# Kernel optimization log

Hardware: AMD Instinct MI355X
Metric: run time of the kernel (lower is better)

The kernel has to match this reference:

```python
import jax, jax.numpy as jnp
import numpy as np

K_SELECTED = 8  # config.num_selected_heads


def setup_inputs() -> dict:
    key = jax.random.key(0)
    k1, k2 = jax.random.split(key, 2)
    B, N, H, L = 4, 4096, 2048, 64
    x = jax.random.normal(k1, (B, N, H), dtype=jnp.float32)
    W_r = jax.random.normal(k2, (L, H), dtype=jnp.float32) * 0.02  # nn.Linear weight (L, H), no bias
    expert_bias = jnp.zeros((L,), dtype=jnp.float32)
    active_mask = jnp.ones((B, N), dtype=bool)
    return {"x": x, "W_r": W_r, "expert_bias": expert_bias, "active_mask": active_mask}


def reference(x, W_r, expert_bias, active_mask):
    L = expert_bias.shape[0]
    K = K_SELECTED
    # logits = x @ W_r.T  (bias-free routing projection)
    logits = jnp.einsum('bnh,lh->bnl', x, W_r)
    routing_scores = jax.nn.softmax(logits, axis=-1)            # unbiased probs
    biased_scores = jax.nn.softmax(logits + expert_bias, -1)    # biased probs for selection
    # top-K on biased scores -> selected head indices (B, N, K)
    _, selected_heads = jax.lax.top_k(biased_scores, K)
    # gather unbiased scores at selected indices and renormalize
    gathered = jnp.take_along_axis(routing_scores, selected_heads, axis=-1)
    routing_probs = gathered / gathered.sum(axis=-1, keepdims=True)
    # scatter into assignment mask: one-hot over L summed over K slots
    assignment_mask = jax.nn.one_hot(selected_heads, L, dtype=x.dtype).sum(axis=-2)  # (B, N, L)
    am = active_mask.astype(x.dtype)
    active_assignments = assignment_mask * am[..., None]
    num_active_assignments = am.sum() * K
    routing_freqs = active_assignments.sum(axis=(0, 1)) / num_active_assignments  # (L,)
    # LoadBalanceLoss.apply(expert_bias, routing_freqs): squared-imbalance value
    inv_L = 1.0 / L
    load_balance_loss = L * jnp.sum((routing_freqs - inv_L) ** 2)
    max_vio = jax.lax.stop_gradient(L * jnp.max(routing_freqs - inv_L))
    return selected_heads, routing_probs, load_balance_loss, max_vio
```

## Files before the change

### kernel.cpp

```cpp
#include <hip/hip_runtime.h>
#include <stdint.h>
#include <math.h>

constexpr int H     = 2048;
constexpr int L     = 64;
constexpr int K_SEL = 8;

constexpr int RPB   = 32;
constexpr int BK    = 32;
constexpr int NSTG  = H / BK;
constexpr int SP    = 40;

constexpr float EPS_GAP = 1e-4f;

constexpr int WS_COUNTS = 0;
constexpr int WS_NFIX   = 128;
constexpr int WS_LIST   = 256;
constexpr int WS_WT     = 16640;
constexpr int WS_WHC    = 147712;
constexpr int WS_WLC    = 213248;

typedef __attribute__((ext_vector_type(8))) short bf16x8;
typedef __attribute__((ext_vector_type(4))) float f32x4;

__device__ __forceinline__ void cvt_hi_lo(float c, short& h, short& l)
{
    unsigned u  = __float_as_uint(c);
    unsigned hb = (u + 0x7fffu + ((u >> 16) & 1u)) >> 16;
    float hf    = __uint_as_float(hb << 16);
    float lof   = c - hf;
    h = (short)hb;
    l = (short)(__float_as_uint(lof) >> 16);
}

__global__ __launch_bounds__(256)
void prep(const float* __restrict__ Wr, float* __restrict__ Wt,
          unsigned int* __restrict__ wsu, short* __restrict__ whc,
          short* __restrict__ wlc)
{
    const int t = threadIdx.x, b = blockIdx.x;
    if (b == 32) {
        if (t < L + 1) wsu[WS_COUNTS + t] = 0u;
        if (t == 0)    wsu[WS_NFIX] = 0u;
        return;
    }
    if (b >= 33) {
        const int z = b - 33;
        const int e = 2 * z + (t >> 7);
        const int idx = t & 127;
        #pragma unroll
        for (int u = 0; u < 4; ++u) {
            const int f4i = idx + 128 * u;
            const int k   = 4 * f4i;
            const float4 v = ((const float4*)(Wr + (size_t)e * H))[f4i];
            short4 hh, ll;
            cvt_hi_lo(v.x, hh.x, ll.x);
            cvt_hi_lo(v.y, hh.y, ll.y);
            cvt_hi_lo(v.z, hh.z, ll.z);
            cvt_hi_lo(v.w, hh.w, ll.w);
            const int c  = k >> 5, kk = k & 31;
            const int di = (c * 64 + e) * 32 + kk;
            *(short4*)(whc + di) = hh;
            *(short4*)(wlc + di) = ll;
        }
        return;
    }
    __shared__ float tile[64 * 65];
    const int k0 = b * 64;
    {
        const int l = t >> 2, kq = (t & 3) * 16;
        #pragma unroll
        for (int j = 0; j < 4; ++j) {
            float4 v = *(const float4*)(Wr + (size_t)l * H + k0 + kq + 4 * j);
            int k = kq + 4 * j;
            tile[(k + 0) * 65 + l] = v.x;
            tile[(k + 1) * 65 + l] = v.y;
            tile[(k + 2) * 65 + l] = v.z;
            tile[(k + 3) * 65 + l] = v.w;
        }
    }
    __syncthreads();
    {
        const int k = t >> 2, lq = (t & 3) * 16;
        #pragma unroll
        for (int j = 0; j < 4; ++j) {
            int l2 = lq + 4 * j;
            float4 o = make_float4(tile[k * 65 + l2], tile[k * 65 + l2 + 1],
                                   tile[k * 65 + l2 + 2], tile[k * 65 + l2 + 3]);
            *(float4*)(Wt + (size_t)(k0 + k) * L + l2) = o;
        }
    }
}

__global__ __launch_bounds__(256, 2)
void router_mfma(const float* __restrict__ x, const short* __restrict__ whc,
                 const short* __restrict__ wlc, const float* __restrict__ bias,
                 const unsigned char* __restrict__ am,
                 float* __restrict__ out_sel, float* __restrict__ out_probs,
                 unsigned int* __restrict__ g_counts, unsigned int* __restrict__ nfix,
                 unsigned int* __restrict__ list)
{
    __shared__ __align__(16) short sxh[2][RPB * SP];
    __shared__ __align__(16) short sxl[2][RPB * SP];
    __shared__ __align__(16) short swh[2][L * SP];
    __shared__ __align__(16) short swl[2][L * SP];
    __shared__ __align__(16) float lg[RPB * 68];
    __shared__ float bs[L];
    __shared__ unsigned int cnt[L + 1];

    const int t  = threadIdx.x;
    const int R0 = blockIdx.x * RPB;

    if (t < L)     bs[t]  = bias[t];
    if (t < L + 1) cnt[t] = 0;

    const int lw  = t & 63, w = t >> 6;
    const int r0l = 16 * (w & 1);
    const int n0  = 32 * (w >> 1);
    const int fr  = lw & 15;
    const int kg  = lw >> 4;
    const int kb  = 8 * kg;

    const float*  xp  = x + (size_t)(R0 + (t >> 3)) * H + 4 * (t & 7);
    const float4* whp = (const float4*)whc + t;
    const float4* wlp = (const float4*)wlc + t;

    f32x4 acc[2] = {};
    float4 xg, wh_r, wl_r;

    xg   = *(const float4*)(xp);
    wh_r = whp[0];
    wl_r = wlp[0];
    {
        short4 h4, l4;
        cvt_hi_lo(xg.x, h4.x, l4.x);
        cvt_hi_lo(xg.y, h4.y, l4.y);
        cvt_hi_lo(xg.z, h4.z, l4.z);
        cvt_hi_lo(xg.w, h4.w, l4.w);
        const int xi = (t >> 3) * SP + 4 * (t & 7);
        *(short4*)&sxh[0][xi] = h4;
        *(short4*)&sxl[0][xi] = l4;
        const int wi = (t >> 2) * SP + 8 * (t & 3);
        *(float4*)&swh[0][wi] = wh_r;
        *(float4*)&swl[0][wi] = wl_r;
    }
    __syncthreads();
    xg   = *(const float4*)(xp + BK);
    wh_r = whp[256];
    wl_r = wlp[256];

    for (int s = 0; s < NSTG; ++s) {
        const int p = s & 1;
        if (s + 1 < NSTG) {
            short4 h4, l4;
            cvt_hi_lo(xg.x, h4.x, l4.x);
            cvt_hi_lo(xg.y, h4.y, l4.y);
            cvt_hi_lo(xg.z, h4.z, l4.z);
            cvt_hi_lo(xg.w, h4.w, l4.w);
            const int xi = (t >> 3) * SP + 4 * (t & 7);
            *(short4*)&sxh[p ^ 1][xi] = h4;
            *(short4*)&sxl[p ^ 1][xi] = l4;
            const int wi = (t >> 2) * SP + 8 * (t & 3);
            *(float4*)&swh[p ^ 1][wi] = wh_r;
            *(float4*)&swl[p ^ 1][wi] = wl_r;
        }
        if (s + 2 < NSTG) {
            xg   = *(const float4*)(xp + BK * (s + 2));
            wh_r = whp[256 * (s + 2)];
            wl_r = wlp[256 * (s + 2)];
        }
        {
            const bf16x8 ah = *(const bf16x8*)&sxh[p][(r0l + fr) * SP + kb];
            const bf16x8 al = *(const bf16x8*)&sxl[p][(r0l + fr) * SP + kb];
            #pragma unroll
            for (int tt = 0; tt < 2; ++tt) {
                const int nc = (n0 + 16 * tt + fr) * SP + kb;
                const bf16x8 bh = *(const bf16x8*)&swh[p][nc];
                const bf16x8 bl = *(const bf16x8*)&swl[p][nc];
                acc[tt] = __builtin_amdgcn_mfma_f32_16x16x32_bf16(ah, bh, acc[tt], 0, 0, 0);
                acc[tt] = __builtin_amdgcn_mfma_f32_16x16x32_bf16(ah, bl, acc[tt], 0, 0, 0);
                acc[tt] = __builtin_amdgcn_mfma_f32_16x16x32_bf16(al, bh, acc[tt], 0, 0, 0);
            }
        }
        __syncthreads();
    }

    #pragma unroll
    for (int tt = 0; tt < 2; ++tt)
        #pragma unroll
        for (int r = 0; r < 4; ++r)
            lg[(r0l + 4 * kg + r) * 68 + n0 + 16 * tt + fr] = acc[tt][r];
    __syncthreads();

    {
        const int tj   = t & 7;
        const int lrow = t >> 3;
        const int grow = R0 + lrow;

        float rv[8], lv[8];
        {
            const float* lp = &lg[lrow * 68 + 8 * tj];
            const float4 v0 = *(const float4*)(lp);
            const float4 v1 = *(const float4*)(lp + 4);
            rv[0] = v0.x; rv[1] = v0.y; rv[2] = v0.z; rv[3] = v0.w;
            rv[4] = v1.x; rv[5] = v1.y; rv[6] = v1.z; rv[7] = v1.w;
            #pragma unroll
            for (int i = 0; i < 8; ++i) lv[i] = rv[i] + bs[8 * tj + i];
        }

        unsigned msk = 0;
        int   selidx[K_SEL];
        float selraw[K_SEL];
        float prev = 0.f, gmin = INFINITY;

        #pragma unroll
        for (int kk = 0; kk < K_SEL + 1; ++kk) {
            float best = -INFINITY; int bi = 1 << 30; float braw = 0.f;
            #pragma unroll
            for (int i = 0; i < 8; ++i) {
                const bool free_ = !((msk >> i) & 1u);
                if (free_ && lv[i] > best) { best = lv[i]; bi = 8 * tj + i; braw = rv[i]; }
            }
            #pragma unroll
            for (int off = 1; off <= 4; off <<= 1) {
                const float ov  = __shfl_xor(best, off);
                const int   oi  = __shfl_xor(bi,   off);
                const float orw = __shfl_xor(braw, off);
                if (ov > best || (ov == best && oi < bi)) { best = ov; bi = oi; braw = orw; }
            }
            if (kk > 0) gmin = fminf(gmin, prev - best);
            prev = best;
            if (kk < K_SEL) {
                if ((bi >> 3) == tj) msk |= 1u << (bi & 7);
                selidx[kk] = bi;
                selraw[kk] = braw;
            }
        }

        if (gmin < EPS_GAP) {
            if (tj == 0) {
                unsigned int pp = atomicAdd(nfix, 1u);
                list[pp] = (unsigned int)grow;
            }
        } else {
            float mx = -INFINITY;
            #pragma unroll
            for (int kk = 0; kk < K_SEL; ++kk) mx = fmaxf(mx, selraw[kk]);
            float e[K_SEL], ssum = 0.f;
            #pragma unroll
            for (int kk = 0; kk < K_SEL; ++kk) { e[kk] = expf(selraw[kk] - mx); ssum += e[kk]; }
            float myp = 0.f; int myi = 0;
            #pragma unroll
            for (int kk = 0; kk < K_SEL; ++kk)
                if (kk == tj) { myp = e[kk] / ssum; myi = selidx[kk]; }
            out_sel  [(size_t)grow * K_SEL + tj] = (float)myi;
            out_probs[(size_t)grow * K_SEL + tj] = myp;
            if (am[grow]) {
                atomicAdd(&cnt[myi], 1u);
                if (tj == 0) atomicAdd(&cnt[L], 1u);
            }
        }
    }
    __syncthreads();
    if (t < L + 1 && cnt[t]) atomicAdd(&g_counts[t], cnt[t]);
}

__global__ __launch_bounds__(256)
void fixup(const float* __restrict__ x, const float* __restrict__ Wt,
           const float* __restrict__ bias, const unsigned char* __restrict__ am,
           const unsigned int* __restrict__ nfix, const unsigned int* __restrict__ list,
           float* __restrict__ out_sel, float* __restrict__ out_probs,
           unsigned int* __restrict__ g_counts)
{
    const int lane = threadIdx.x & 63;
    const int wid  = (blockIdx.x << 2) | (threadIdx.x >> 6);
    const int nw   = gridDim.x << 2;
    const int n    = (int)*nfix;
    const double bl = (double)bias[lane];

    for (int i = wid; i < n; i += nw) {
        const int row = (int)list[i];
        const float* xr = x + (size_t)row * H;
        double a0 = 0.0, a1 = 0.0, a2 = 0.0, a3 = 0.0;
        #pragma unroll 2
        for (int k = 0; k < H; k += 16) {
            float4 x0 = *(const float4*)(xr + k);
            float4 x1 = *(const float4*)(xr + k + 4);
            float4 x2 = *(const float4*)(xr + k + 8);
            float4 x3 = *(const float4*)(xr + k + 12);
            a0 = fma((double)x0.x, (double)Wt[(k +  0) * L + lane], a0);
            a1 = fma((double)x0.y, (double)Wt[(k +  1) * L + lane], a1);
            a2 = fma((double)x0.z, (double)Wt[(k +  2) * L + lane], a2);
            a3 = fma((double)x0.w, (double)Wt[(k +  3) * L + lane], a3);
            a0 = fma((double)x1.x, (double)Wt[(k +  4) * L + lane], a0);
            a1 = fma((double)x1.y, (double)Wt[(k +  5) * L + lane], a1);
            a2 = fma((double)x1.z, (double)Wt[(k +  6) * L + lane], a2);
            a3 = fma((double)x1.w, (double)Wt[(k +  7) * L + lane], a3);
            a0 = fma((double)x2.x, (double)Wt[(k +  8) * L + lane], a0);
            a1 = fma((double)x2.y, (double)Wt[(k +  9) * L + lane], a1);
            a2 = fma((double)x2.z, (double)Wt[(k + 10) * L + lane], a2);
            a3 = fma((double)x2.w, (double)Wt[(k + 11) * L + lane], a3);
            a0 = fma((double)x3.x, (double)Wt[(k + 12) * L + lane], a0);
            a1 = fma((double)x3.y, (double)Wt[(k + 13) * L + lane], a1);
            a2 = fma((double)x3.z, (double)Wt[(k + 14) * L + lane], a2);
            a3 = fma((double)x3.w, (double)Wt[(k + 15) * L + lane], a3);
        }
        double acc = (a0 + a1) + (a2 + a3);

        double v = acc + bl;
        int    widx[K_SEL];
        double wlog[K_SEL];
        #pragma unroll
        for (int kk = 0; kk < K_SEL; ++kk) {
            double mv = v; int mi = lane;
            #pragma unroll
            for (int off = 32; off; off >>= 1) {
                double ov = __shfl_xor(mv, off);
                int    oi = __shfl_xor(mi, off);
                if (ov > mv || (ov == mv && oi < mi)) { mv = ov; mi = oi; }
            }
            widx[kk] = mi;
            wlog[kk] = __shfl(acc, mi);
            if (lane == mi) v = -INFINITY;
        }

        double mx = -INFINITY;
        #pragma unroll
        for (int kk = 0; kk < K_SEL; ++kk) mx = fmax(mx, wlog[kk]);
        float e[K_SEL], ssum = 0.f;
        #pragma unroll
        for (int kk = 0; kk < K_SEL; ++kk) { e[kk] = expf((float)(wlog[kk] - mx)); ssum += e[kk]; }

        if (lane < K_SEL) {
            out_sel[(size_t)row * K_SEL + lane]   = (float)widx[lane];
            out_probs[(size_t)row * K_SEL + lane] = e[lane] / ssum;
        }
        if (am[row]) {
            if (lane < K_SEL)  atomicAdd(&g_counts[widx[lane]], 1u);
            if (lane == K_SEL) atomicAdd(&g_counts[L], 1u);
        }
    }
}

__global__ void router_finalize(const unsigned int* __restrict__ g_counts,
                                float* __restrict__ out_scalars)
{
    const int l = threadIdx.x;
    const float denom = (float)g_counts[L] * (float)K_SEL;
    const float f = (float)g_counts[l] / denom;
    float d  = f - 1.0f / (float)L;
    float sq = d * d;
    #pragma unroll
    for (int o = 32; o > 0; o >>= 1) {
        sq += __shfl_down(sq, o);
        d = fmaxf(d, __shfl_down(d, o));
    }
    if (l == 0) {
        out_scalars[0] = (float)L * sq;
        out_scalars[1] = (float)L * d;
    }
}

extern "C" void kernel_launch(void* const* d_in, const int* in_sizes, int n_in,
                              void* d_out, int out_size, void* d_ws, size_t ws_size,
                              hipStream_t stream)
{
    const float* x          = (const float*)d_in[0];
    const float* Wr         = (const float*)d_in[1];
    const float* bias       = (const float*)d_in[2];
    const unsigned char* am = (const unsigned char*)d_in[3];
    float* out = (float*)d_out;
    float* wsf = (float*)d_ws;
    unsigned int* wsu = (unsigned int*)d_ws;

    const int rows = in_sizes[3];

    float* out_sel   = out;
    float* out_probs = out + (size_t)rows * K_SEL;
    float* out_scal  = out + (size_t)rows * K_SEL * 2;

    short* whc = (short*)(wsu + WS_WHC);
    short* wlc = (short*)(wsu + WS_WLC);

    hipLaunchKernelGGL(prep,            dim3(65),         dim3(256), 0, stream,
                       Wr, wsf + WS_WT, wsu, whc, wlc);
    hipLaunchKernelGGL(router_mfma,     dim3(rows / RPB), dim3(256), 0, stream,
                       x, whc, wlc, bias, am, out_sel, out_probs,
                       wsu + WS_COUNTS, wsu + WS_NFIX, wsu + WS_LIST);
    hipLaunchKernelGGL(fixup,           dim3(256),        dim3(256), 0, stream,
                       x, wsf + WS_WT, bias, am, wsu + WS_NFIX, wsu + WS_LIST,
                       out_sel, out_probs, wsu + WS_COUNTS);
    hipLaunchKernelGGL(router_finalize, dim3(1),          dim3(64),  0, stream,
                       wsu + WS_COUNTS, out_scal);
}
```

Before: 281.2 us.

## Split-K across waves with direct register loads and fuse finalize into fixup

The MFMA router kernel drops its shared-memory double-buffered staging. Each of the four waves now loads x and the pre-split bf16 weight fragments straight from global memory into registers for its own quarter of H, computes the full 32x64 tile, and the four partial tiles are summed in LDS. This removes the per-stage barriers and LDS traffic but quadruples weight fragment loads and uses more registers. Separately, the finalize kernel is folded into the fixup kernel through a last-block-done atomic counter, saving a launch.

```diff
diff --git a/kernel.cpp b/kernel.cpp
--- a/kernel.cpp
+++ b/kernel.cpp
@@ -7,14 +7,13 @@
 constexpr int K_SEL = 8;
 
 constexpr int RPB   = 32;
-constexpr int BK    = 32;
-constexpr int NSTG  = H / BK;
-constexpr int SP    = 40;
+constexpr int NCH   = 16;
 
 constexpr float EPS_GAP = 1e-4f;
 
 constexpr int WS_COUNTS = 0;
 constexpr int WS_NFIX   = 128;
+constexpr int WS_DONE   = 192;
 constexpr int WS_LIST   = 256;
 constexpr int WS_WT     = 16640;
 constexpr int WS_WHC    = 147712;
@@ -33,6 +32,29 @@
     l = (short)(__float_as_uint(lof) >> 16);
 }
 
+__device__ __forceinline__ void cvt8(const float4& u0, const float4& u1,
+                                     bf16x8& h, bf16x8& l)
+{
+    short hh, ll;
+    cvt_hi_lo(u0.x, hh, ll); h[0] = hh; l[0] = ll;
+    cvt_hi_lo(u0.y, hh, ll); h[1] = hh; l[1] = ll;
+    cvt_hi_lo(u0.z, hh, ll); h[2] = hh; l[2] = ll;
+    cvt_hi_lo(u0.w, hh, ll); h[3] = hh; l[3] = ll;
+    cvt_hi_lo(u1.x, hh, ll); h[4] = hh; l[4] = ll;
+    cvt_hi_lo(u1.y, hh, ll); h[5] = hh; l[5] = ll;
+    cvt_hi_lo(u1.z, hh, ll); h[6] = hh; l[6] = ll;
+    cvt_hi_lo(u1.w, hh, ll); h[7] = hh; l[7] = ll;
+}
+
+__device__ __forceinline__ f32x4 mm3(const bf16x8& ah, const bf16x8& al,
+                                     const bf16x8& bh, const bf16x8& bl, f32x4 c)
+{
+    c = __builtin_amdgcn_mfma_f32_16x16x32_bf16(ah, bh, c, 0, 0, 0);
+    c = __builtin_amdgcn_mfma_f32_16x16x32_bf16(ah, bl, c, 0, 0, 0);
+    c = __builtin_amdgcn_mfma_f32_16x16x32_bf16(al, bh, c, 0, 0, 0);
+    return c;
+}
+
 __global__ __launch_bounds__(256)
 void prep(const float* __restrict__ Wr, float* __restrict__ Wt,
           unsigned int* __restrict__ wsu, short* __restrict__ whc,
@@ -42,6 +64,7 @@
     if (b == 32) {
         if (t < L + 1) wsu[WS_COUNTS + t] = 0u;
         if (t == 0)    wsu[WS_NFIX] = 0u;
+        if (t == 1)    wsu[WS_DONE] = 0u;
         return;
     }
     if (b >= 33) {
@@ -100,96 +123,85 @@
                  unsigned int* __restrict__ g_counts, unsigned int* __restrict__ nfix,
                  unsigned int* __restrict__ list)
 {
-    __shared__ __align__(16) short sxh[2][RPB * SP];
-    __shared__ __align__(16) short sxl[2][RPB * SP];
-    __shared__ __align__(16) short swh[2][L * SP];
-    __shared__ __align__(16) short swl[2][L * SP];
-    __shared__ __align__(16) float lg[RPB * 68];
+    __shared__ __align__(16) float lg[4 * RPB * 68];
     __shared__ float bs[L];
     __shared__ unsigned int cnt[L + 1];
 
     const int t  = threadIdx.x;
     const int R0 = blockIdx.x * RPB;
+    const int w  = t >> 6, l = t & 63;
+    const int fr = l & 15;
+    const int kg = l >> 4;
+    const int kb = 8 * kg;
 
     if (t < L)     bs[t]  = bias[t];
     if (t < L + 1) cnt[t] = 0;
 
-    const int lw  = t & 63, w = t >> 6;
-    const int r0l = 16 * (w & 1);
-    const int n0  = 32 * (w >> 1);
-    const int fr  = lw & 15;
-    const int kg  = lw >> 4;
-    const int kb  = 8 * kg;
-
-    const float*  xp  = x + (size_t)(R0 + (t >> 3)) * H + 4 * (t & 7);
-    const float4* whp = (const float4*)whc + t;
-    const float4* wlp = (const float4*)wlc + t;
-
-    f32x4 acc[2] = {};
-    float4 xg, wh_r, wl_r;
-
-    xg   = *(const float4*)(xp);
-    wh_r = whp[0];
-    wl_r = wlp[0];
+    f32x4 acc_00 = {}, acc_01 = {}, acc_02 = {}, acc_03 = {};
+    f32x4 acc_10 = {}, acc_11 = {}, acc_12 = {}, acc_13 = {};
+
+    const float* xp0 = x + (size_t)(R0 + fr) * H + kb;
+    const float* xp1 = xp0 + (size_t)16 * H;
+    const short* whp = whc + fr * 32 + kb;
+    const short* wlp = wlc + fr * 32 + kb;
+
+    #pragma unroll
+    for (int ci = 0; ci < NCH; ++ci) {
+        const int c  = NCH * w + ci;
+        const int xo = 32 * c;
+        const int wo = c * 2048;
+
+        const float4 a00 = *(const float4*)(xp0 + xo);
+        const float4 a01 = *(const float4*)(xp0 + xo + 4);
+        const float4 a10 = *(const float4*)(xp1 + xo);
+        const float4 a11 = *(const float4*)(xp1 + xo + 4);
+
+        const bf16x8 bh0 = *(const bf16x8*)(whp + wo);
+        const bf16x8 bh1 = *(const bf16x8*)(whp + wo + 512);
+        const bf16x8 bh2 = *(const bf16x8*)(whp + wo + 1024);
+        const bf16x8 bh3 = *(const bf16x8*)(whp + wo + 1536);
+        const bf16x8 bl0 = *(const bf16x8*)(wlp + wo);
+        const bf16x8 bl1 = *(const bf16x8*)(wlp + wo + 512);
+        const bf16x8 bl2 = *(const bf16x8*)(wlp + wo + 1024);
+        const bf16x8 bl3 = *(const bf16x8*)(wlp + wo + 1536);
+
+        bf16x8 ah0, al0, ah1, al1;
+        cvt8(a00, a01, ah0, al0);
+        cvt8(a10, a11, ah1, al1);
+
+        acc_00 = mm3(ah0, al0, bh0, bl0, acc_00);
+        acc_01 = mm3(ah0, al0, bh1, bl1, acc_01);
+        acc_02 = mm3(ah0, al0, bh2, bl2, acc_02);
+        acc_03 = mm3(ah0, al0, bh3, bl3, acc_03);
+        acc_10 = mm3(ah1, al1, bh0, bl0, acc_10);
+        acc_11 = mm3(ah1, al1, bh1, bl1, acc_11);
+        acc_12 = mm3(ah1, al1, bh2, bl2, acc_12);
+        acc_13 = mm3(ah1, al1, bh3, bl3, acc_13);
+    }
+
     {
-        short4 h4, l4;
-        cvt_hi_lo(xg.x, h4.x, l4.x);
-        cvt_hi_lo(xg.y, h4.y, l4.y);
-        cvt_hi_lo(xg.z, h4.z, l4.z);
-        cvt_hi_lo(xg.w, h4.w, l4.w);
-        const int xi = (t >> 3) * SP + 4 * (t & 7);
-        *(short4*)&sxh[0][xi] = h4;
-        *(short4*)&sxl[0][xi] = l4;
-        const int wi = (t >> 2) * SP + 8 * (t & 3);
-        *(float4*)&swh[0][wi] = wh_r;
-        *(float4*)&swl[0][wi] = wl_r;
-    }
-    __syncthreads();
-    xg   = *(const float4*)(xp + BK);
-    wh_r = whp[256];
-    wl_r = wlp[256];
-
-    for (int s = 0; s < NSTG; ++s) {
-        const int p = s & 1;
-        if (s + 1 < NSTG) {
-            short4 h4, l4;
-            cvt_hi_lo(xg.x, h4.x, l4.x);
-            cvt_hi_lo(xg.y, h4.y, l4.y);
-            cvt_hi_lo(xg.z, h4.z, l4.z);
-            cvt_hi_lo(xg.w, h4.w, l4.w);
-            const int xi = (t >> 3) * SP + 4 * (t & 7);
-            *(short4*)&sxh[p ^ 1][xi] = h4;
-            *(short4*)&sxl[p ^ 1][xi] = l4;
-            const int wi = (t >> 2) * SP + 8 * (t & 3);
-            *(float4*)&swh[p ^ 1][wi] = wh_r;
-            *(float4*)&swl[p ^ 1][wi] = wl_r;
-        }
-        if (s + 2 < NSTG) {
-            xg   = *(const float4*)(xp + BK * (s + 2));
-            wh_r = whp[256 * (s + 2)];
-            wl_r = wlp[256 * (s + 2)];
-        }
-        {
-            const bf16x8 ah = *(const bf16x8*)&sxh[p][(r0l + fr) * SP + kb];
-            const bf16x8 al = *(const bf16x8*)&sxl[p][(r0l + fr) * SP + kb];
-            #pragma unroll
-            for (int tt = 0; tt < 2; ++tt) {
-                const int nc = (n0 + 16 * tt + fr) * SP + kb;
-                const bf16x8 bh = *(const bf16x8*)&swh[p][nc];
-                const bf16x8 bl = *(const bf16x8*)&swl[p][nc];
-                acc[tt] = __builtin_amdgcn_mfma_f32_16x16x32_bf16(ah, bh, acc[tt], 0, 0, 0);
-                acc[tt] = __builtin_amdgcn_mfma_f32_16x16x32_bf16(ah, bl, acc[tt], 0, 0, 0);
-                acc[tt] = __builtin_amdgcn_mfma_f32_16x16x32_bf16(al, bh, acc[tt], 0, 0, 0);
-            }
-        }
-        __syncthreads();
-    }
+        float* lgw = lg + w * (RPB * 68);
+        const int rb = 4 * kg;
+        #pragma unroll
+        for (int r = 0; r < 4; ++r) {
+            lgw[(rb + r)      * 68 + fr     ] = acc_00[r];
+            lgw[(rb + r)      * 68 + fr + 16] = acc_01[r];
+            lgw[(rb + r)      * 68 + fr + 32] = acc_02[r];
+            lgw[(rb + r)      * 68 + fr + 48] = acc_03[r];
+            lgw[(rb + r + 16) * 68 + fr     ] = acc_10[r];
+            lgw[(rb + r + 16) * 68 + fr + 16] = acc_11[r];
+            lgw[(rb + r + 16) * 68 + fr + 32] = acc_12[r];
+            lgw[(rb + r + 16) * 68 + fr + 48] = acc_13[r];
+        }
+    }
+    __syncthreads();
 
     #pragma unroll
-    for (int tt = 0; tt < 2; ++tt)
-        #pragma unroll
-        for (int r = 0; r < 4; ++r)
-            lg[(r0l + 4 * kg + r) * 68 + n0 + 16 * tt + fr] = acc[tt][r];
+    for (int q = 0; q < 9; ++q) {
+        const int p = t + 256 * q;
+        if (p < RPB * 68)
+            lg[p] = (lg[p] + lg[RPB * 68 + p]) + (lg[2 * RPB * 68 + p] + lg[3 * RPB * 68 + p]);
+    }
     __syncthreads();
 
     {
@@ -266,11 +278,12 @@
 }
 
 __global__ __launch_bounds__(256)
-void fixup(const float* __restrict__ x, const float* __restrict__ Wt,
-           const float* __restrict__ bias, const unsigned char* __restrict__ am,
-           const unsigned int* __restrict__ nfix, const unsigned int* __restrict__ list,
-           float* __restrict__ out_sel, float* __restrict__ out_probs,
-           unsigned int* __restrict__ g_counts)
+void fixup_fin(const float* __restrict__ x, const float* __restrict__ Wt,
+               const float* __restrict__ bias, const unsigned char* __restrict__ am,
+               const unsigned int* __restrict__ nfix, const unsigned int* __restrict__ list,
+               float* __restrict__ out_sel, float* __restrict__ out_probs,
+               unsigned int* __restrict__ g_counts, unsigned int* __restrict__ done,
+               float* __restrict__ out_scalars)
 {
     const int lane = threadIdx.x & 63;
     const int wid  = (blockIdx.x << 2) | (threadIdx.x >> 6);
@@ -340,24 +353,33 @@
             if (lane == K_SEL) atomicAdd(&g_counts[L], 1u);
         }
     }
-}
-
-__global__ void router_finalize(const unsigned int* __restrict__ g_counts,
-                                float* __restrict__ out_scalars)
-{
+
+    __shared__ bool last;
+    __syncthreads();
+    if (threadIdx.x == 0) {
+        __threadfence();
+        last = (atomicAdd(done, 1u) == (unsigned)gridDim.x - 1u);
+    }
+    __syncthreads();
+    if (!last) return;
+
     const int l = threadIdx.x;
-    const float denom = (float)g_counts[L] * (float)K_SEL;
-    const float f = (float)g_counts[l] / denom;
-    float d  = f - 1.0f / (float)L;
-    float sq = d * d;
-    #pragma unroll
-    for (int o = 32; o > 0; o >>= 1) {
-        sq += __shfl_down(sq, o);
-        d = fmaxf(d, __shfl_down(d, o));
-    }
-    if (l == 0) {
-        out_scalars[0] = (float)L * sq;
-        out_scalars[1] = (float)L * d;
+    if (l < L) {
+        const unsigned cl = atomicAdd(&g_counts[l], 0u);
+        const unsigned ct = atomicAdd(&g_counts[L], 0u);
+        const float denom = (float)ct * (float)K_SEL;
+        const float f = (float)cl / denom;
+        float d  = f - 1.0f / (float)L;
+        float sq = d * d;
+        #pragma unroll
+        for (int o = 32; o > 0; o >>= 1) {
+            sq += __shfl_down(sq, o);
+            d = fmaxf(d, __shfl_down(d, o));
+        }
+        if (l == 0) {
+            out_scalars[0] = (float)L * sq;
+            out_scalars[1] = (float)L * d;
+        }
     }
 }
 
@@ -382,14 +404,13 @@
     short* whc = (short*)(wsu + WS_WHC);
     short* wlc = (short*)(wsu + WS_WLC);
 
-    hipLaunchKernelGGL(prep,            dim3(65),         dim3(256), 0, stream,
+    hipLaunchKernelGGL(prep,        dim3(65),         dim3(256), 0, stream,
                        Wr, wsf + WS_WT, wsu, whc, wlc);
-    hipLaunchKernelGGL(router_mfma,     dim3(rows / RPB), dim3(256), 0, stream,
+    hipLaunchKernelGGL(router_mfma, dim3(rows / RPB), dim3(256), 0, stream,
                        x, whc, wlc, bias, am, out_sel, out_probs,
                        wsu + WS_COUNTS, wsu + WS_NFIX, wsu + WS_LIST);
-    hipLaunchKernelGGL(fixup,           dim3(256),        dim3(256), 0, stream,
+    hipLaunchKernelGGL(fixup_fin,   dim3(256),        dim3(256), 0, stream,
                        x, wsf + WS_WT, bias, am, wsu + WS_NFIX, wsu + WS_LIST,
-                       out_sel, out_probs, wsu + WS_COUNTS);
-    hipLaunchKernelGGL(router_finalize, dim3(1),          dim3(64),  0, stream,
-                       wsu + WS_COUNTS, out_scal);
-}
+                       out_sel, out_probs, wsu + WS_COUNTS, wsu + WS_DONE,
+                       out_scal);
+}
```

After: 270.9 us. 3.7% less time.
